# Performance work log

Hardware: AMD Instinct MI355X
Metric: run time of the kernel (lower is better)

Reference implementation:

```python
import jax, jax.numpy as jnp
import numpy as np

N_E = 1024
E_DIM = 256
N_TOK = 131072


def setup_inputs() -> dict:
    key = jax.random.key(0)
    kz, kw = jax.random.split(key)
    z = jax.random.normal(kz, (N_TOK, E_DIM), dtype=jnp.float32)
    weight = jax.random.normal(kw, (N_E, E_DIM), dtype=jnp.float32)
    return {"z": z, "weight": weight}


def reference(z, weight):
    # squared L2 distances: ||z||^2 + ||e||^2 - 2 z e^T  -> [N, n_e]
    d = (jnp.sum(z * z, axis=1, keepdims=True)
         + jnp.sum(weight * weight, axis=1)
         - 2.0 * jnp.matmul(z, weight.T))
    idx = jnp.argmin(d, axis=1)                       # [N]
    # gather codebook rows instead of materializing the one-hot @ weight matmul
    z_q = weight[idx]                                 # [N, e_dim]
    # straight-through estimator
    z_q = z + jax.lax.stop_gradient(z_q - z)
    # e_mean = mean of one-hot encodings == normalized code counts
    counts = jax.ops.segment_sum(jnp.ones_like(idx, dtype=z.dtype), idx,
                                 num_segments=N_E)    # [n_e]
    e_mean = counts / z.shape[0]
    perplexity = jnp.exp(-jnp.sum(e_mean * jnp.log(e_mean + 1e-10)))
    return z_q, perplexity
```

## Files before the change

kernel.cpp:

```cpp
#include <hip/hip_runtime.h>
#include <math.h>

#define NE   1024
#define ED   256
#define NT   131072
#define SLOTS 32

typedef __attribute__((ext_vector_type(8))) short short8;
typedef __attribute__((ext_vector_type(4))) float f32x4;

__device__ inline unsigned short f2bf(float f) {
    unsigned u = __float_as_uint(f);
    unsigned r = (u + 0x7FFFu + ((u >> 16) & 1u)) >> 16;
    return (unsigned short)r;
}

__device__ inline void gl_lds16(const void* g, void* l) {
    __builtin_amdgcn_global_load_lds(
        (const __attribute__((address_space(1))) unsigned int*)g,
        (__attribute__((address_space(3))) unsigned int*)l, 16, 0, 0);
}

__device__ inline unsigned pack_cand(float s, int code) {
    float qf = (s + 1024.f) * 16.f;
    int q = (int)qf;
    q = q < 0 ? 0 : (q > 65535 ? 65535 : q);
    return ((unsigned)q << 16) | (unsigned)code;
}


__global__ __launch_bounds__(256) void vq_prep(const float* __restrict__ w,
                                               float* __restrict__ wnorm,
                                               int* __restrict__ counts,
                                               unsigned short* __restrict__ wb) {
    int c = blockIdx.x * 256 + threadIdx.x;
    if (c < NE) {
        const float4* row = reinterpret_cast<const float4*>(w + (size_t)c * ED);
        ushort4* wbr = reinterpret_cast<ushort4*>(wb + (size_t)c * ED);
        float s = 0.f;
#pragma unroll 8
        for (int i = 0; i < ED / 4; ++i) {
            float4 v = row[i];
            s += v.x * v.x + v.y * v.y + v.z * v.z + v.w * v.w;
            ushort4 o;
            o.x = f2bf(v.x); o.y = f2bf(v.y); o.z = f2bf(v.z); o.w = f2bf(v.w);
            wbr[i] = o;
        }
        wnorm[c] = s;
        counts[c] = 0;
    }
}

__global__ __launch_bounds__(1024) void vq_wmax(const float* __restrict__ wnorm,
                                                float* __restrict__ wmax) {
    __shared__ float red[16];
    int tid = threadIdx.x;
    float v = wnorm[tid];
#pragma unroll
    for (int m = 32; m >= 1; m >>= 1) v = fmaxf(v, __shfl_xor(v, m, 64));
    if ((tid & 63) == 0) red[tid >> 6] = v;
    __syncthreads();
    if (tid == 0) {
        float m = red[0];
#pragma unroll
        for (int i = 1; i < 16; ++i) m = fmaxf(m, red[i]);
        wmax[0] = sqrtf(m);
    }
}

__global__ __launch_bounds__(256) void vq_score3(const float* __restrict__ z,
                                                 const unsigned short* __restrict__ wb,
                                                 const float* __restrict__ wnorm,
                                                 const float* __restrict__ wmaxp,
                                                 unsigned* __restrict__ cnt,
                                                 unsigned* __restrict__ cand) {
    __shared__ __align__(16) unsigned short wlds[16384];
    __shared__ float wn_lds[NE];
    __shared__ float thr_lds[4][32];

    const int tid  = threadIdx.x;
    const int lane = tid & 63;
    const int wv_  = tid >> 6;
    const int l15  = lane & 15;
    const int l4   = lane >> 4;
    const int row0 = blockIdx.x * 128 + wv_ * 32;

#pragma unroll
    for (int p = 0; p < 8; ++p) {
        int s  = wv_ * 8 + p;
        int nj = s >> 3, kg = s & 7;
        int j  = nj * 16 + l15;
        gl_lds16(wb + (size_t)j * ED + kg * 32 + l4 * 8, &wlds[s * 512]);
    }

    reinterpret_cast<float4*>(wn_lds)[tid] = reinterpret_cast<const float4*>(wnorm)[tid];

    short8 a[2][8];
    float zn2[2];
#pragma unroll
    for (int mi = 0; mi < 2; ++mi) {
        const float* zr = z + (size_t)(row0 + mi * 16 + l15) * ED;
        float s = 0.f;
#pragma unroll
        for (int kg = 0; kg < 8; ++kg) {
            int k0 = kg * 32 + l4 * 8;
            float4 p = *reinterpret_cast<const float4*>(zr + k0);
            float4 q = *reinterpret_cast<const float4*>(zr + k0 + 4);
            s += p.x * p.x + p.y * p.y + p.z * p.z + p.w * p.w
               + q.x * q.x + q.y * q.y + q.z * q.z + q.w * q.w;
            short8 t;
            t[0] = (short)f2bf(p.x); t[1] = (short)f2bf(p.y);
            t[2] = (short)f2bf(p.z); t[3] = (short)f2bf(p.w);
            t[4] = (short)f2bf(q.x); t[5] = (short)f2bf(q.y);
            t[6] = (short)f2bf(q.z); t[7] = (short)f2bf(q.w);
            a[mi][kg] = t;
        }
        zn2[mi] = s;
    }
#pragma unroll
    for (int mi = 0; mi < 2; ++mi) {
        zn2[mi] += __shfl_xor(zn2[mi], 16, 64);
        zn2[mi] += __shfl_xor(zn2[mi], 32, 64);
    }
    float wmax = wmaxp[0];
#pragma unroll
    for (int mi = 0; mi < 2; ++mi)
        thr_lds[wv_][mi * 16 + l15] = 0.0313f * sqrtf(zn2[mi]) * wmax + 0.05f;

    asm volatile("s_waitcnt vmcnt(0) lgkmcnt(0)" ::: "memory");
    __builtin_amdgcn_s_barrier();

    float thrR[2], mn[2];
    int cnt_reg[2];
#pragma unroll
    for (int mi = 0; mi < 2; ++mi) {
        thrR[mi] = thr_lds[wv_][mi * 16 + l15];
        mn[mi] = 3.4e38f;
        cnt_reg[mi] = 0;
    }

    for (int st = 0; st < 16; ++st) {
        const int c0 = st * 64;

        for (int base = 0; base < 4; base += 2) {
            f32x4 acc[2][2];
#pragma unroll
            for (int tb = 0; tb < 2; ++tb)
#pragma unroll
                for (int mi = 0; mi < 2; ++mi) acc[tb][mi] = {0.f, 0.f, 0.f, 0.f};

#pragma unroll
            for (int tb = 0; tb < 2; ++tb)
#pragma unroll
                for (int kg = 0; kg < 8; ++kg) {
                    short8 wf = *reinterpret_cast<const short8*>(
                        &wlds[(((base + tb) * 8 + kg) * 512) + lane * 8]);
                    acc[tb][0] = __builtin_amdgcn_mfma_f32_16x16x32_bf16(wf, a[0][kg], acc[tb][0], 0, 0, 0);
                    acc[tb][1] = __builtin_amdgcn_mfma_f32_16x16x32_bf16(wf, a[1][kg], acc[tb][1], 0, 0, 0);
                }

            float4 wnv[2];
#pragma unroll
            for (int tb = 0; tb < 2; ++tb)
                wnv[tb] = *reinterpret_cast<const float4*>(
                    &wn_lds[c0 + (base + tb) * 16 + l4 * 4]);

            float tmin[2] = {3.4e38f, 3.4e38f};
#pragma unroll
            for (int tb = 0; tb < 2; ++tb)
#pragma unroll
                for (int mi = 0; mi < 2; ++mi) {
                    float wr[4] = {wnv[tb].x, wnv[tb].y, wnv[tb].z, wnv[tb].w};
#pragma unroll
                    for (int r = 0; r < 4; ++r) {
                        float s = fmaf(-2.f, acc[tb][mi][r], wr[r]);
                        acc[tb][mi][r] = s;
                        tmin[mi] = fminf(tmin[mi], s);
                    }
                }
#pragma unroll
            for (int mi = 0; mi < 2; ++mi) {
                float v = tmin[mi];
                v = fminf(v, __shfl_xor(v, 16, 64));
                v = fminf(v, __shfl_xor(v, 32, 64));
                mn[mi] = fminf(mn[mi], v);
            }

            unsigned km[2] = {0u, 0u};
#pragma unroll
            for (int tb = 0; tb < 2; ++tb)
#pragma unroll
                for (int mi = 0; mi < 2; ++mi)
#pragma unroll
                    for (int r = 0; r < 4; ++r)
                        if (acc[tb][mi][r] <= mn[mi] + thrR[mi])
                            km[mi] |= 1u << (tb * 4 + r);

            if (__any((km[0] | km[1]) != 0u)) {
#pragma unroll
                for (int mi = 0; mi < 2; ++mi) {
                    int kc = __popc(km[mi]);
                    int b = __shfl_xor(kc, 16, 64);
                    int c = __shfl_xor(kc, 32, 64);
                    int d = __shfl_xor(b, 32, 64);
                    int tot = kc + b + c + d;
                    if (tot > 0) {
                        int pfx = (l4 == 1) ? b
                                : (l4 == 2) ? (c + d)
                                : (l4 == 3) ? (b + c + d) : 0;
                        int tok = row0 + mi * 16 + l15;
                        int o = 0;
#pragma unroll
                        for (int tb = 0; tb < 2; ++tb)
#pragma unroll
                            for (int r = 0; r < 4; ++r)
                                if (km[mi] & (1u << (tb * 4 + r))) {
                                    int pos = cnt_reg[mi] + pfx + o;
                                    if (pos < SLOTS)
                                        cand[(size_t)tok * SLOTS + pos] =
                                            pack_cand(acc[tb][mi][r],
                                                      c0 + (base + tb) * 16 + l4 * 4 + r);
                                    ++o;
                                }
                        cnt_reg[mi] += tot;
                    }
                }
            }
        }

        if (st < 15) {
            asm volatile("s_waitcnt lgkmcnt(0)" ::: "memory");
            __builtin_amdgcn_s_barrier();
#pragma unroll
            for (int p = 0; p < 8; ++p) {
                int s  = wv_ * 8 + p;
                int nj = s >> 3, kg = s & 7;
                int j  = (st + 1) * 64 + nj * 16 + l15;
                gl_lds16(wb + (size_t)j * ED + kg * 32 + l4 * 8, &wlds[s * 512]);
            }
            asm volatile("s_waitcnt vmcnt(0) lgkmcnt(0)" ::: "memory");
            __builtin_amdgcn_s_barrier();
        }
    }

    if (l4 == 0) {
        cnt[row0 + l15]      = (unsigned)cnt_reg[0];
        cnt[row0 + 16 + l15] = (unsigned)cnt_reg[1];
    }
}

__global__ __launch_bounds__(256) void vq_refine(const float* __restrict__ z,
                                                 const float* __restrict__ w,
                                                 const float* __restrict__ wnorm,
                                                 const float* __restrict__ wmaxp,
                                                 const unsigned* __restrict__ cnt,
                                                 const unsigned* __restrict__ cand,
                                                 int* __restrict__ counts,
                                                 float* __restrict__ out) {
    const int lane = threadIdx.x & 63;
    const int t = blockIdx.x * 4 + (threadIdx.x >> 6);
    float4 zv = reinterpret_cast<const float4*>(z + (size_t)t * ED)[lane];
    unsigned n = cnt[t];
    float bs = 3.4e38f;
    int bj = NE;

    if (n >= 1u && n <= (unsigned)SLOTS) {
        unsigned pk = 0xFFFFFFFFu;
        if (lane < (int)n) pk = cand[(size_t)t * SLOTS + lane];
        unsigned pmin = pk;
#pragma unroll
        for (int m = 1; m < 64; m <<= 1) {
            unsigned o = __shfl_xor(pmin, m, 64);
            pmin = o < pmin ? o : pmin;
        }
        float zn = zv.x * zv.x + zv.y * zv.y + zv.z * zv.z + zv.w * zv.w;
#pragma unroll
        for (int m = 1; m < 64; m <<= 1) zn += __shfl_xor(zn, m, 64);
        float thr = 0.0313f * sqrtf(zn) * wmaxp[0] + 0.05f;
        unsigned margin = (unsigned)(16.f * thr) + 2u;
        unsigned qmin = pmin >> 16;
        bool keep = (lane < (int)n) && ((pk >> 16) <= qmin + margin);
        unsigned long long mask = __ballot(keep);
        while (mask) {
            int c = __ffsll(mask) - 1;
            mask &= mask - 1;
            int j = (int)(__shfl(pk, c, 64) & 0xFFFFu);
            float4 wv = reinterpret_cast<const float4*>(w + (size_t)j * ED)[lane];
            float d = fmaf(zv.x, wv.x, fmaf(zv.y, wv.y, fmaf(zv.z, wv.z, zv.w * wv.w)));
#pragma unroll
            for (int m = 1; m < 64; m <<= 1) d += __shfl_xor(d, m, 64);
            float s = fmaf(-2.f, d, wnorm[j]);
            if (s < bs || (s == bs && j < bj)) { bs = s; bj = j; }
        }
    } else {
        for (int j = 0; j < NE; ++j) {
            float4 wv = reinterpret_cast<const float4*>(w + (size_t)j * ED)[lane];
            float d = fmaf(zv.x, wv.x, fmaf(zv.y, wv.y, fmaf(zv.z, wv.z, zv.w * wv.w)));
#pragma unroll
            for (int m = 1; m < 64; m <<= 1) d += __shfl_xor(d, m, 64);
            float s = fmaf(-2.f, d, wnorm[j]);
            if (s < bs || (s == bs && j < bj)) { bs = s; bj = j; }
        }
    }
    float4 bw = reinterpret_cast<const float4*>(w + (size_t)bj * ED)[lane];
    reinterpret_cast<float4*>(out + (size_t)t * ED)[lane] = bw;
    if (lane == 0) atomicAdd(&counts[bj], 1);
}

__global__ __launch_bounds__(1024) void vq_pplx(const int* __restrict__ counts,
                                                float* __restrict__ out) {
    __shared__ float red[16];
    int tid = threadIdx.x;
    float e = (float)counts[tid] * (1.0f / (float)NT);
    float t = -e * logf(e + 1e-10f);
#pragma unroll
    for (int m = 32; m >= 1; m >>= 1) t += __shfl_down(t, m, 64);
    if ((tid & 63) == 0) red[tid >> 6] = t;
    __syncthreads();
    if (tid < 16) {
        float s = red[tid];
#pragma unroll
        for (int m = 8; m >= 1; m >>= 1) s += __shfl_down(s, m, 16);
        if (tid == 0) out[(size_t)NT * ED] = expf(s);
    }
}

#define TM 64
#define TN 64
#define KC 64

__global__ __launch_bounds__(256) void vq_prep0(const float* __restrict__ w,
                                                float* __restrict__ wnorm,
                                                int* __restrict__ counts) {
    int c = blockIdx.x * blockDim.x + threadIdx.x;
    if (c < NE) {
        const float4* row = reinterpret_cast<const float4*>(w + (size_t)c * ED);
        float s = 0.f;
#pragma unroll 8
        for (int i = 0; i < ED / 4; ++i) {
            float4 v = row[i];
            s += v.x * v.x + v.y * v.y + v.z * v.z + v.w * v.w;
        }
        wnorm[c] = s;
        counts[c] = 0;
    }
}

__global__ __launch_bounds__(256) void vq_argmin0(const float* __restrict__ z,
                                                  const float* __restrict__ w,
                                                  const float* __restrict__ wnorm,
                                                  int* __restrict__ idx_out,
                                                  int* __restrict__ counts) {
    __shared__ float zs[ED][TM];
    __shared__ float wsh[KC][TN];
    const int tid  = threadIdx.x;
    const int row0 = blockIdx.x * TM;
    const int cg   = tid & 15;
    const int tg   = tid >> 4;
#pragma unroll
    for (int p = 0; p < 16; ++p) {
        int f = p * 256 + tid;
        int k = f >> 4;
        int g = f & 15;
        float4 v;
        v.x = z[(size_t)(row0 + g * 4 + 0) * ED + k];
        v.y = z[(size_t)(row0 + g * 4 + 1) * ED + k];
        v.z = z[(size_t)(row0 + g * 4 + 2) * ED + k];
        v.w = z[(size_t)(row0 + g * 4 + 3) * ED + k];
        *reinterpret_cast<float4*>(&zs[k][g * 4]) = v;
    }
    float best[4];
    int   bidx[4];
#pragma unroll
    for (int i = 0; i < 4; ++i) { best[i] = 3.4e38f; bidx[i] = 0; }
    for (int ct = 0; ct < NE / TN; ++ct) {
        const int c0 = ct * TN;
        float acc[4][4];
#pragma unroll
        for (int i = 0; i < 4; ++i)
#pragma unroll
            for (int j = 0; j < 4; ++j) acc[i][j] = 0.f;
        for (int kc = 0; kc < ED / KC; ++kc) {
            __syncthreads();
#pragma unroll
            for (int p = 0; p < 4; ++p) {
                int f = p * 256 + tid;
                int k = f >> 4;
                int g = f & 15;
                float4 v;
                v.x = w[(size_t)(c0 + g * 4 + 0) * ED + kc * KC + k];
                v.y = w[(size_t)(c0 + g * 4 + 1) * ED + kc * KC + k];
                v.z = w[(size_t)(c0 + g * 4 + 2) * ED + kc * KC + k];
                v.w = w[(size_t)(c0 + g * 4 + 3) * ED + kc * KC + k];
                *reinterpret_cast<float4*>(&wsh[k][g * 4]) = v;
            }
            __syncthreads();
#pragma unroll 8
            for (int k = 0; k < KC; ++k) {
                float4 zv = *reinterpret_cast<const float4*>(&zs[kc * KC + k][tg * 4]);
                float4 wv = *reinterpret_cast<const float4*>(&wsh[k][cg * 4]);
                float zr[4] = { zv.x, zv.y, zv.z, zv.w };
                float wr[4] = { wv.x, wv.y, wv.z, wv.w };
#pragma unroll
                for (int i = 0; i < 4; ++i)
#pragma unroll
                    for (int j = 0; j < 4; ++j)
                        acc[i][j] = fmaf(zr[i], wr[j], acc[i][j]);
            }
        }
#pragma unroll
        for (int j = 0; j < 4; ++j) {
            int c = c0 + cg * 4 + j;
            float wn = wnorm[c];
#pragma unroll
            for (int i = 0; i < 4; ++i) {
                float s = fmaf(-2.f, acc[i][j], wn);
                if (s < best[i]) { best[i] = s; bidx[i] = c; }
            }
        }
    }
#pragma unroll
    for (int m = 1; m < 16; m <<= 1) {
#pragma unroll
        for (int i = 0; i < 4; ++i) {
            float ov = __shfl_xor(best[i], m, 64);
            int   oi = __shfl_xor(bidx[i], m, 64);
            if (ov < best[i] || (ov == best[i] && oi < bidx[i])) {
                best[i] = ov; bidx[i] = oi;
            }
        }
    }
    if (cg == 0) {
#pragma unroll
        for (int i = 0; i < 4; ++i) {
            int t = row0 + tg * 4 + i;
            idx_out[t] = bidx[i];
            atomicAdd(&counts[bidx[i]], 1);
        }
    }
}

__global__ __launch_bounds__(256) void vq_gather0(const float* __restrict__ w,
                                                  const int* __restrict__ idx,
                                                  float* __restrict__ out) {
    int tid = threadIdx.x;
    int t   = blockIdx.x * 4 + (tid >> 6);
    int c4  = tid & 63;
    int id  = idx[t];
    float4 v = reinterpret_cast<const float4*>(w + (size_t)id * ED)[c4];
    reinterpret_cast<float4*>(out + (size_t)t * ED)[c4] = v;
}

extern "C" void kernel_launch(void* const* d_in, const int* in_sizes, int n_in,
                              void* d_out, int out_size, void* d_ws, size_t ws_size,
                              hipStream_t stream) {
    const float* z = (const float*)d_in[0];
    const float* w = (const float*)d_in[1];
    float* out = (float*)d_out;
    char* ws = (char*)d_ws;

    float*          wnorm  = (float*)ws;
    int*            counts = (int*)(ws + 4096);
    float*          wmax   = (float*)(ws + 8192);
    unsigned short* wb     = (unsigned short*)(ws + 8448);
    unsigned*       cnt    = (unsigned*)(ws + 532736);
    unsigned*       cand   = (unsigned*)(ws + 1057024);
    const size_t need = 1057024 + (size_t)NT * SLOTS * 4;

    if (ws_size >= need) {
        vq_prep<<<4, 256, 0, stream>>>(w, wnorm, counts, wb);
        vq_wmax<<<1, 1024, 0, stream>>>(wnorm, wmax);
        vq_score3<<<NT / 128, 256, 0, stream>>>(z, wb, wnorm, wmax, cnt, cand);
        vq_refine<<<NT / 4, 256, 0, stream>>>(z, w, wnorm, wmax, cnt, cand, counts, out);
        vq_pplx<<<1, 1024, 0, stream>>>(counts, out);
    } else {
        int* idxw = (int*)(ws + 8192);
        vq_prep0<<<(NE + 255) / 256, 256, 0, stream>>>(w, wnorm, counts);
        vq_argmin0<<<NT / TM, 256, 0, stream>>>(z, w, wnorm, idxw, counts);
        vq_gather0<<<NT / 4, 256, 0, stream>>>(w, idxw, out);
        vq_pplx<<<1, 1024, 0, stream>>>(counts, out);
    }
}
```

Baseline: 286.2 us.

## Double per-wave token tile to reuse codebook LDS fragments and tighten candidate threshold

The scoring kernel now processes 64 tokens per wave (256 per block) instead of 32, so each bf16 codebook fragment read from LDS feeds four MFMAs instead of two. This halves the grid and the number of times the whole codebook is staged through LDS. The candidate-pruning threshold is also tightened (relative and absolute margins roughly halved), which should leave fewer candidates for the fp32 refine kernel to check. Costs: more VGPRs for A fragments and accumulators, which may lower occupancy. The tighter bf16 error margin also risks dropping the true argmin.

```diff
diff --git a/kernel.cpp b/kernel.cpp
--- a/kernel.cpp
+++ b/kernel.cpp
@@ -5,6 +5,9 @@
 #define ED   256
 #define NT   131072
 #define SLOTS 32
+
+#define THR_REL 0.016f
+#define THR_ABS 0.02f
 
 typedef __attribute__((ext_vector_type(8))) short short8;
 typedef __attribute__((ext_vector_type(4))) float f32x4;
@@ -68,7 +71,7 @@
     }
 }
 
-__global__ __launch_bounds__(256) void vq_score3(const float* __restrict__ z,
+__global__ __launch_bounds__(256) void vq_score5(const float* __restrict__ z,
                                                  const unsigned short* __restrict__ wb,
                                                  const float* __restrict__ wnorm,
                                                  const float* __restrict__ wmaxp,
@@ -76,14 +79,13 @@
                                                  unsigned* __restrict__ cand) {
     __shared__ __align__(16) unsigned short wlds[16384];
     __shared__ float wn_lds[NE];
-    __shared__ float thr_lds[4][32];
 
     const int tid  = threadIdx.x;
     const int lane = tid & 63;
     const int wv_  = tid >> 6;
     const int l15  = lane & 15;
     const int l4   = lane >> 4;
-    const int row0 = blockIdx.x * 128 + wv_ * 32;
+    const int row0 = blockIdx.x * 256 + wv_ * 64;
 
 #pragma unroll
     for (int p = 0; p < 8; ++p) {
@@ -95,59 +97,49 @@
 
     reinterpret_cast<float4*>(wn_lds)[tid] = reinterpret_cast<const float4*>(wnorm)[tid];
 
-    short8 a[2][8];
-    float zn2[2];
-#pragma unroll
-    for (int mi = 0; mi < 2; ++mi) {
-        const float* zr = z + (size_t)(row0 + mi * 16 + l15) * ED;
-        float s = 0.f;
-#pragma unroll
-        for (int kg = 0; kg < 8; ++kg) {
-            int k0 = kg * 32 + l4 * 8;
-            float4 p = *reinterpret_cast<const float4*>(zr + k0);
-            float4 q = *reinterpret_cast<const float4*>(zr + k0 + 4);
-            s += p.x * p.x + p.y * p.y + p.z * p.z + p.w * p.w
-               + q.x * q.x + q.y * q.y + q.z * q.z + q.w * q.w;
-            short8 t;
-            t[0] = (short)f2bf(p.x); t[1] = (short)f2bf(p.y);
-            t[2] = (short)f2bf(p.z); t[3] = (short)f2bf(p.w);
-            t[4] = (short)f2bf(q.x); t[5] = (short)f2bf(q.y);
-            t[6] = (short)f2bf(q.z); t[7] = (short)f2bf(q.w);
-            a[mi][kg] = t;
-        }
-        zn2[mi] = s;
-    }
-#pragma unroll
-    for (int mi = 0; mi < 2; ++mi) {
-        zn2[mi] += __shfl_xor(zn2[mi], 16, 64);
-        zn2[mi] += __shfl_xor(zn2[mi], 32, 64);
-    }
-    float wmax = wmaxp[0];
-#pragma unroll
-    for (int mi = 0; mi < 2; ++mi)
-        thr_lds[wv_][mi * 16 + l15] = 0.0313f * sqrtf(zn2[mi]) * wmax + 0.05f;
+    short8 a[4][8];
+    float thrR[4], mn[4];
+    int cnt_reg[4];
+    {
+        float wmax = wmaxp[0];
+#pragma unroll
+        for (int mi = 0; mi < 4; ++mi) {
+            const float* zr = z + (size_t)(row0 + mi * 16 + l15) * ED;
+            float s = 0.f;
+#pragma unroll
+            for (int kg = 0; kg < 8; ++kg) {
+                int k0 = kg * 32 + l4 * 8;
+                float4 p = *reinterpret_cast<const float4*>(zr + k0);
+                float4 q = *reinterpret_cast<const float4*>(zr + k0 + 4);
+                s += p.x * p.x + p.y * p.y + p.z * p.z + p.w * p.w
+                   + q.x * q.x + q.y * q.y + q.z * q.z + q.w * q.w;
+                short8 t;
+                t[0] = (short)f2bf(p.x); t[1] = (short)f2bf(p.y);
+                t[2] = (short)f2bf(p.z); t[3] = (short)f2bf(p.w);
+                t[4] = (short)f2bf(q.x); t[5] = (short)f2bf(q.y);
+                t[6] = (short)f2bf(q.z); t[7] = (short)f2bf(q.w);
+                a[mi][kg] = t;
+            }
+            s += __shfl_xor(s, 16, 64);
+            s += __shfl_xor(s, 32, 64);
+            thrR[mi] = THR_REL * sqrtf(s) * wmax + THR_ABS;
+            mn[mi] = 3.4e38f;
+            cnt_reg[mi] = 0;
+        }
+    }
 
     asm volatile("s_waitcnt vmcnt(0) lgkmcnt(0)" ::: "memory");
     __builtin_amdgcn_s_barrier();
 
-    float thrR[2], mn[2];
-    int cnt_reg[2];
-#pragma unroll
-    for (int mi = 0; mi < 2; ++mi) {
-        thrR[mi] = thr_lds[wv_][mi * 16 + l15];
-        mn[mi] = 3.4e38f;
-        cnt_reg[mi] = 0;
-    }
-
     for (int st = 0; st < 16; ++st) {
         const int c0 = st * 64;
 
         for (int base = 0; base < 4; base += 2) {
-            f32x4 acc[2][2];
+            f32x4 acc[2][4];
 #pragma unroll
             for (int tb = 0; tb < 2; ++tb)
 #pragma unroll
-                for (int mi = 0; mi < 2; ++mi) acc[tb][mi] = {0.f, 0.f, 0.f, 0.f};
+                for (int mi = 0; mi < 4; ++mi) acc[tb][mi] = {0.f, 0.f, 0.f, 0.f};
 
 #pragma unroll
             for (int tb = 0; tb < 2; ++tb)
@@ -157,6 +149,8 @@
                         &wlds[(((base + tb) * 8 + kg) * 512) + lane * 8]);
                     acc[tb][0] = __builtin_amdgcn_mfma_f32_16x16x32_bf16(wf, a[0][kg], acc[tb][0], 0, 0, 0);
                     acc[tb][1] = __builtin_amdgcn_mfma_f32_16x16x32_bf16(wf, a[1][kg], acc[tb][1], 0, 0, 0);
+                    acc[tb][2] = __builtin_amdgcn_mfma_f32_16x16x32_bf16(wf, a[2][kg], acc[tb][2], 0, 0, 0);
+                    acc[tb][3] = __builtin_amdgcn_mfma_f32_16x16x32_bf16(wf, a[3][kg], acc[tb][3], 0, 0, 0);
                 }
 
             float4 wnv[2];
@@ -165,40 +159,40 @@
                 wnv[tb] = *reinterpret_cast<const float4*>(
                     &wn_lds[c0 + (base + tb) * 16 + l4 * 4]);
 
-            float tmin[2] = {3.4e38f, 3.4e38f};
-#pragma unroll
-            for (int tb = 0; tb < 2; ++tb)
-#pragma unroll
-                for (int mi = 0; mi < 2; ++mi) {
-                    float wr[4] = {wnv[tb].x, wnv[tb].y, wnv[tb].z, wnv[tb].w};
+            float tmin[4] = {3.4e38f, 3.4e38f, 3.4e38f, 3.4e38f};
+#pragma unroll
+            for (int tb = 0; tb < 2; ++tb) {
+                float wr[4] = {wnv[tb].x, wnv[tb].y, wnv[tb].z, wnv[tb].w};
+#pragma unroll
+                for (int mi = 0; mi < 4; ++mi)
 #pragma unroll
                     for (int r = 0; r < 4; ++r) {
                         float s = fmaf(-2.f, acc[tb][mi][r], wr[r]);
                         acc[tb][mi][r] = s;
                         tmin[mi] = fminf(tmin[mi], s);
                     }
-                }
-#pragma unroll
-            for (int mi = 0; mi < 2; ++mi) {
+            }
+#pragma unroll
+            for (int mi = 0; mi < 4; ++mi) {
                 float v = tmin[mi];
                 v = fminf(v, __shfl_xor(v, 16, 64));
                 v = fminf(v, __shfl_xor(v, 32, 64));
                 mn[mi] = fminf(mn[mi], v);
             }
 
-            unsigned km[2] = {0u, 0u};
+            unsigned km[4] = {0u, 0u, 0u, 0u};
 #pragma unroll
             for (int tb = 0; tb < 2; ++tb)
 #pragma unroll
-                for (int mi = 0; mi < 2; ++mi)
+                for (int mi = 0; mi < 4; ++mi)
 #pragma unroll
                     for (int r = 0; r < 4; ++r)
                         if (acc[tb][mi][r] <= mn[mi] + thrR[mi])
                             km[mi] |= 1u << (tb * 4 + r);
 
-            if (__any((km[0] | km[1]) != 0u)) {
-#pragma unroll
-                for (int mi = 0; mi < 2; ++mi) {
+            if (__any((km[0] | km[1] | km[2] | km[3]) != 0u)) {
+#pragma unroll
+                for (int mi = 0; mi < 4; ++mi) {
                     int kc = __popc(km[mi]);
                     int b = __shfl_xor(kc, 16, 64);
                     int c = __shfl_xor(kc, 32, 64);
@@ -244,8 +238,9 @@
     }
 
     if (l4 == 0) {
-        cnt[row0 + l15]      = (unsigned)cnt_reg[0];
-        cnt[row0 + 16 + l15] = (unsigned)cnt_reg[1];
+#pragma unroll
+        for (int mi = 0; mi < 4; ++mi)
+            cnt[row0 + mi * 16 + l15] = (unsigned)cnt_reg[mi];
     }
 }
 
@@ -276,7 +271,7 @@
         float zn = zv.x * zv.x + zv.y * zv.y + zv.z * zv.z + zv.w * zv.w;
 #pragma unroll
         for (int m = 1; m < 64; m <<= 1) zn += __shfl_xor(zn, m, 64);
-        float thr = 0.0313f * sqrtf(zn) * wmaxp[0] + 0.05f;
+        float thr = THR_REL * sqrtf(zn) * wmaxp[0] + THR_ABS;
         unsigned margin = (unsigned)(16.f * thr) + 2u;
         unsigned qmin = pmin >> 16;
         bool keep = (lane < (int)n) && ((pk >> 16) <= qmin + margin);
@@ -470,7 +465,7 @@
     if (ws_size >= need) {
         vq_prep<<<4, 256, 0, stream>>>(w, wnorm, counts, wb);
         vq_wmax<<<1, 1024, 0, stream>>>(wnorm, wmax);
-        vq_score3<<<NT / 128, 256, 0, stream>>>(z, wb, wnorm, wmax, cnt, cand);
+        vq_score5<<<NT / 256, 256, 0, stream>>>(z, wb, wnorm, wmax, cnt, cand);
         vq_refine<<<NT / 4, 256, 0, stream>>>(z, w, wnorm, wmax, cnt, cand, counts, out);
         vq_pplx<<<1, 1024, 0, stream>>>(counts, out);
     } else {
```

Result: slower. 356.2 us (+24.5%).
